# Kernel optimization log

Measured on AMD Instinct MI355X. Metric: run time of the kernel, lower is better.

The kernel has to match this reference:

```python
import math
import jax, jax.numpy as jnp
import numpy as np

B, S, D = 4, 2048, 512
N_HEADS, D_HEAD = 8, 64
NUM_BUCKETS, MAX_DIST = 32, 128


def _relative_position_bucket(relative_position, num_buckets=NUM_BUCKETS, max_distance=MAX_DIST):
    # bidirectional variant (is_decoder=False)
    num_buckets = num_buckets // 2
    rel_buckets = (relative_position > 0).astype(jnp.int32) * num_buckets
    rp = jnp.abs(relative_position)
    max_exact = num_buckets // 2
    is_small = rp < max_exact
    rp_large = max_exact + (
        jnp.log(rp.astype(jnp.float32) / max_exact)
        / math.log(max_distance / max_exact)
        * (num_buckets - max_exact)
    ).astype(jnp.int32)
    rp_large = jnp.minimum(rp_large, num_buckets - 1)
    return rel_buckets + jnp.where(is_small, rp, rp_large)


def compute_bias(rel_bias, q_len, k_len):
    ctx = jnp.arange(q_len)[:, None]
    mem = jnp.arange(k_len)[None, :]
    buckets = _relative_position_bucket(mem - ctx)           # [q, k]
    values = rel_bias[buckets]                                # [q, k, h]
    return jnp.transpose(values, (2, 0, 1))[None]             # [1, h, q, k]


def setup_inputs() -> dict:
    key = jax.random.key(0)
    ks = jax.random.split(key, 6)
    scale = 1.0 / math.sqrt(D)
    return {
        "hidden_states": jax.random.normal(ks[0], (B, S, D), jnp.float32),
        "Wq": jax.random.normal(ks[1], (D, D), jnp.float32) * scale,
        "Wk": jax.random.normal(ks[2], (D, D), jnp.float32) * scale,
        "Wv": jax.random.normal(ks[3], (D, D), jnp.float32) * scale,
        "Wo": jax.random.normal(ks[4], (D, D), jnp.float32) * scale,
        "rel_bias": jax.random.normal(ks[5], (NUM_BUCKETS, N_HEADS), jnp.float32),
    }


def reference(hidden_states, Wq, Wk, Wv, Wo, rel_bias):
    b, s, _ = hidden_states.shape
    # projections (no bias, no 1/sqrt(d) scaling — T5 style)
    q = (hidden_states @ Wq).reshape(b, s, N_HEADS, D_HEAD).transpose(0, 2, 1, 3)
    k = (hidden_states @ Wk).reshape(b, s, N_HEADS, D_HEAD).transpose(0, 2, 1, 3)
    v = (hidden_states @ Wv).reshape(b, s, N_HEADS, D_HEAD).transpose(0, 2, 1, 3)
    scores = jnp.einsum("bhqd,bhkd->bhqk", q, k)             # [b,h,s,s]
    position_bias = compute_bias(rel_bias, s, s)              # [1,h,s,s]
    scores = scores + position_bias
    attn = jax.nn.softmax(scores, axis=-1)                    # dropout: eval mode -> identity
    out = jnp.einsum("bhqk,bhkd->bhqd", attn, v)
    out = out.transpose(0, 2, 1, 3).reshape(b, s, N_HEADS * D_HEAD)
    return out @ Wo
```

## Files before the change

kernel.cpp:

```cpp
#include <hip/hip_runtime.h>
#include <stdint.h>

typedef __attribute__((ext_vector_type(8))) __bf16 bf16x8;
typedef __attribute__((ext_vector_type(4))) __bf16 bf16x4;
typedef __attribute__((ext_vector_type(8))) _Float16 f16x8;
typedef __attribute__((ext_vector_type(4))) float f32x4;
typedef __attribute__((ext_vector_type(4))) unsigned int u32x4;

#define SEQ 2048
#define LOG2E 1.4426950408889634f

#define OFF_AO    0ull
#define OFF_WF    8388608ull
#define OFF_WO    9961472ull
#define OFF_Q     10485760ull
#define OFF_K     18874368ull
#define OFF_VT    27262976ull
#define OFF_BIAS  35651584ull

__device__ __forceinline__ int swz(int row) { return ((row & 7) << 4) ^ ((row & 8) << 1); }

__device__ __forceinline__ void gl_lds16(const void* g, void* l) {
  __builtin_amdgcn_global_load_lds(
      (__attribute__((address_space(1))) void*)(uintptr_t)g,
      (__attribute__((address_space(3))) void*)(uint32_t)(uintptr_t)l, 16, 0, 0);
}

__device__ __forceinline__ float fast_exp2(float x) { return __builtin_amdgcn_exp2f(x); }

__global__ void k_prep(const float* __restrict__ Wq, const float* __restrict__ Wk,
                       const float* __restrict__ Wv, const float* __restrict__ Wo,
                       const float* __restrict__ rel_bias,
                       _Float16* __restrict__ wf, __bf16* __restrict__ wo_t,
                       float* __restrict__ bias_tab) {
  int z = blockIdx.z;
  __shared__ float tile[64][65];
  const float* W = (z == 0) ? Wq : (z == 1) ? Wk : (z == 2) ? Wv : Wo;
  int k0 = blockIdx.y * 64, n0 = blockIdx.x * 64;
  int tx = threadIdx.x & 63, ty = threadIdx.x >> 6;
  for (int r = ty; r < 64; r += 4) tile[r][tx] = W[(size_t)(k0 + r) * 512 + n0 + tx];
  __syncthreads();
  if (z < 3) {
    float scale = (z == 0) ? LOG2E : 1.0f;
    for (int r = ty; r < 64; r += 4)
      wf[(size_t)(z * 512 + n0 + r) * 512 + k0 + tx] = (_Float16)(tile[tx][r] * scale);
  } else {
    for (int r = ty; r < 64; r += 4)
      wo_t[(size_t)(n0 + r) * 512 + k0 + tx] = (__bf16)tile[tx][r];
    int blk = blockIdx.y * 8 + blockIdx.x;
#pragma unroll
    for (int e = 0; e < 2; ++e) {
      int idx = blk * 512 + e * 256 + threadIdx.x;
      int h = idx >> 12, dIdx = idx & 4095;
      float v = 0.f;
      if (dIdx < 4095) {
        int d = dIdx - 2047;
        int rp = d < 0 ? -d : d;
        int bp;
        if (rp < 8) bp = rp;
        else bp = 8 + (rp >= 12) + (rp >= 16) + (rp >= 23) + (rp >= 32) + (rp >= 46) + (rp >= 64) + (rp >= 91);
        v = rel_bias[((d > 0 ? 16 : 0) + bp) * 8 + h] * LOG2E;
      }
      bias_tab[idx] = v;
    }
  }
}

template <int MODE, int KSTEPS, int LDA, int LDB>
__global__ __launch_bounds__(256) void k_gemm(const void* __restrict__ Ap,
                                              const void* __restrict__ Btp,
                                              _Float16* __restrict__ qf,
                                              _Float16* __restrict__ kf,
                                              __bf16* __restrict__ vt,
                                              float* __restrict__ fo) {
  __shared__ __align__(16) char As[2][128 * 32 * 2];
  __shared__ __align__(16) char Bs[2][128 * 32 * 2];
  int tid = threadIdx.x, w = tid >> 6, l = tid & 63;
  int lr = l & 15, lh = l >> 4;
  int nwg = gridDim.x * gridDim.y;
  int flat = blockIdx.y * gridDim.x + blockIdx.x;
  int flat2 = (flat & 7) * (nwg >> 3) + (flat >> 3);
  int m0 = (flat2 / gridDim.x) * 128, n0 = (flat2 % gridDim.x) * 128;
  int wm = (w >> 1) * 64, wn = (w & 1) * 64;
  f32x4 zero4 = {0.f, 0.f, 0.f, 0.f};
  f32x4 acc[4][4];
#pragma unroll
  for (int i = 0; i < 4; ++i)
#pragma unroll
    for (int j = 0; j < 4; ++j) acc[i][j] = zero4;

  auto stage = [&](int kt, int buf) {
    if (MODE == 0) {
      const float* Af = (const float*)Ap;
#pragma unroll
      for (int c = 0; c < 2; ++c) {
        int i = c * 256 + tid;
        int row = i >> 2, cc = i & 3;
        const float* src = Af + (size_t)(m0 + row) * LDA + kt * 32 + cc * 8;
        float4 a = *(const float4*)src, b2 = *(const float4*)(src + 4);
        f16x8 hv;
        hv[0] = (_Float16)a.x;  hv[1] = (_Float16)a.y;
        hv[2] = (_Float16)a.z;  hv[3] = (_Float16)a.w;
        hv[4] = (_Float16)b2.x; hv[5] = (_Float16)b2.y;
        hv[6] = (_Float16)b2.z; hv[7] = (_Float16)b2.w;
        *(f16x8*)&As[buf][i * 16] = hv;
      }
#pragma unroll
      for (int c = 0; c < 2; ++c) {
        int i = c * 256 + tid;
        int row = i >> 2, cc = i & 3;
        gl_lds16((const char*)Btp + ((size_t)(n0 + row) * LDB + kt * 32 + cc * 8) * 2,
                 &Bs[buf][i * 16]);
      }
    } else {
#pragma unroll
      for (int c = 0; c < 2; ++c) {
        int i = c * 256 + tid;
        int row = i >> 2, cc = i & 3;
        gl_lds16((const char*)Ap + ((size_t)(m0 + row) * LDA + kt * 32 + cc * 8) * 2,
                 &As[buf][i * 16]);
        gl_lds16((const char*)Btp + ((size_t)(n0 + row) * LDB + kt * 32 + cc * 8) * 2,
                 &Bs[buf][i * 16]);
      }
    }
  };

  stage(0, 0);
  __syncthreads();
#pragma unroll 2
  for (int kt = 0; kt < KSTEPS; ++kt) {
    int cur = kt & 1;
    if (kt + 1 < KSTEPS) stage(kt + 1, cur ^ 1);
    u32x4 af[4], bfr[4];
#pragma unroll
    for (int mi = 0; mi < 4; ++mi)
      af[mi] = *(const u32x4*)&As[cur][((wm + mi * 16 + lr) * 32 + lh * 8) * 2];
#pragma unroll
    for (int ni = 0; ni < 4; ++ni)
      bfr[ni] = *(const u32x4*)&Bs[cur][((wn + ni * 16 + lr) * 32 + lh * 8) * 2];
#pragma unroll
    for (int mi = 0; mi < 4; ++mi)
#pragma unroll
      for (int ni = 0; ni < 4; ++ni) {
        if (MODE == 0)
          acc[mi][ni] = __builtin_amdgcn_mfma_f32_16x16x32_f16(
              __builtin_bit_cast(f16x8, af[mi]), __builtin_bit_cast(f16x8, bfr[ni]),
              acc[mi][ni], 0, 0, 0);
        else
          acc[mi][ni] = __builtin_amdgcn_mfma_f32_16x16x32_bf16(
              __builtin_bit_cast(bf16x8, af[mi]), __builtin_bit_cast(bf16x8, bfr[ni]),
              acc[mi][ni], 0, 0, 0);
      }
    __syncthreads();
  }

  if (MODE == 0 && n0 >= 1024) {
#pragma unroll
    for (int mi = 0; mi < 4; ++mi)
#pragma unroll
      for (int ni = 0; ni < 4; ++ni) {
        int m = m0 + wm + mi * 16 + lh * 4;
        int n = n0 + wn + ni * 16 + lr;
        int c9 = n & 511, hh = c9 >> 6, dh = c9 & 63;
        int b = m >> 11, s = m & 2047;
        int loc = s & 63;
        int pp = ((loc >> 5) << 5) | (((loc >> 2) & 3) << 3) | (((loc >> 4) & 1) << 2);
        bf16x4 o;
#pragma unroll
        for (int r = 0; r < 4; ++r) o[r] = (__bf16)acc[mi][ni][r];
        *(bf16x4*)&vt[((size_t)(b * 8 + hh) * 64 + dh) * 2048 + (s & ~63) + pp] = o;
      }
    return;
  }

#pragma unroll
  for (int mi = 0; mi < 4; ++mi)
#pragma unroll
    for (int ni = 0; ni < 4; ++ni)
#pragma unroll
      for (int r = 0; r < 4; ++r) {
        int m = m0 + wm + mi * 16 + lh * 4 + r;
        int n = n0 + wn + ni * 16 + lr;
        float vv = acc[mi][ni][r];
        if (MODE == 0) {
          int which = n >> 9, c9 = n & 511, hh = c9 >> 6, dh = c9 & 63;
          int b = m >> 11, s = m & 2047;
          size_t o = (size_t)((b * 8 + hh) * 2048 + s) * 64 + dh;
          if (which == 0) qf[o] = (_Float16)vv;
          else            kf[o] = (_Float16)vv;
        } else {
          fo[(size_t)m * 512 + n] = vv;
        }
      }
}

__global__ __launch_bounds__(512) void k_attn(const _Float16* __restrict__ qfp,
                                              const _Float16* __restrict__ kfp,
                                              const __bf16* __restrict__ vt,
                                              const float* __restrict__ bias_tab,
                                              __bf16* __restrict__ ao) {
  __shared__ __align__(16) char Ks[4][64 * 128];
  __shared__ __align__(16) char Vs[4][64 * 128];
  __shared__ float bias_s[2304];
  int tid = threadIdx.x, w = tid >> 6, l = tid & 63;
  int lr = l & 15, lh = l >> 4;
  int d = blockIdx.x;
  int bh = (d & 7) + ((d >> 3) & 3) * 8;
  int q0 = (d >> 5) * 256;
  int h = bh & 7, b = bh >> 3;
  const char* kbase = (const char*)(kfp + (size_t)bh * SEQ * 64);
  const char* vbase = (const char*)(vt + (size_t)bh * 64 * SEQ);

  float bR = bias_tab[h * 4096 + 2047 + 200];
  float bL = bias_tab[h * 4096 + 2047 - 200];

  for (int j = tid; j < 2304; j += 512)
    bias_s[j] = bias_tab[h * 4096 + (1792 - q0) + j];

  auto stageKV = [&](int kt, int buf) {
    const char* kb = kbase + (size_t)kt * 64 * 128;
    const char* vb = vbase + (size_t)kt * 128;
    int row = tid >> 3, colb = (tid & 7) * 16;
    gl_lds16(kb + row * 128 + (colb ^ swz(row)), &Ks[buf][tid * 16]);
    gl_lds16(vb + (size_t)row * 4096 + (colb ^ swz(row)), &Vs[buf][tid * 16]);
  };

  f16x8 qf[2][2];
#pragma unroll
  for (int qs = 0; qs < 2; ++qs) {
    int qrow = w * 32 + qs * 16 + lr;
    const _Float16* qg = qfp + ((size_t)bh * SEQ + q0 + qrow) * 64;
    qf[qs][0] = *(const f16x8*)(qg + lh * 8);
    qf[qs][1] = *(const f16x8*)(qg + 32 + lh * 8);
  }

  float l_run0 = 0.f, l_run1 = 0.f;
  f32x4 zero4 = {0.f, 0.f, 0.f, 0.f};
  f32x4 oacc[2][4];
#pragma unroll
  for (int qs = 0; qs < 2; ++qs)
#pragma unroll
    for (int i = 0; i < 4; ++i) oacc[qs][i] = zero4;

  auto qk = [&](int kt, int buf, f32x4 (&sacc)[2][4]) {
    int dmin = kt * 64 - q0 - 255, dmax = kt * 64 + 63 - q0;
    bool far = (dmin >= 91) || (dmax <= -91);
    f32x4 cinit[2][4];
    if (far) {
      float cb = (dmin >= 91) ? bR : bL;
#pragma unroll
      for (int qs = 0; qs < 2; ++qs)
#pragma unroll
        for (int t = 0; t < 4; ++t)
#pragma unroll
          for (int r = 0; r < 4; ++r) cinit[qs][t][r] = cb;
    } else {
#pragma unroll
      for (int qs = 0; qs < 2; ++qs) {
        int jb = kt * 64 + lh * 4 + 255 - (w * 32 + qs * 16 + lr);
#pragma unroll
        for (int t = 0; t < 4; ++t)
#pragma unroll
          for (int r = 0; r < 4; ++r) cinit[qs][t][r] = bias_s[jb + t * 16 + r];
      }
    }
    const char* kb = &Ks[buf][0];
    __builtin_amdgcn_s_setprio(1);
#pragma unroll
    for (int t = 0; t < 4; ++t) {
      int row = t * 16 + lr;
      f16x8 b0 = *(const f16x8*)(kb + row * 128 + ((lh * 16) ^ swz(row)));
      f16x8 b1 = *(const f16x8*)(kb + row * 128 + ((64 + lh * 16) ^ swz(row)));
#pragma unroll
      for (int qs = 0; qs < 2; ++qs) {
        f32x4 z = cinit[qs][t];
        z = __builtin_amdgcn_mfma_f32_16x16x32_f16(b0, qf[qs][0], z, 0, 0, 0);
        z = __builtin_amdgcn_mfma_f32_16x16x32_f16(b1, qf[qs][1], z, 0, 0, 0);
        sacc[qs][t] = z;
      }
    }
    __builtin_amdgcn_s_setprio(0);
  };

  auto finish = [&](int buf, f32x4 (&sacc)[2][4]) {
    bf16x8 paA[2], paB[2];
#pragma unroll
    for (int qs = 0; qs < 2; ++qs) {
      float p[4][4];
      float rt[4];
#pragma unroll
      for (int t = 0; t < 4; ++t) {
#pragma unroll
        for (int r = 0; r < 4; ++r) p[t][r] = fast_exp2(sacc[qs][t][r]);
        rt[t] = (p[t][0] + p[t][1]) + (p[t][2] + p[t][3]);
      }
      if (qs == 0) l_run0 += (rt[0] + rt[1]) + (rt[2] + rt[3]);
      else         l_run1 += (rt[0] + rt[1]) + (rt[2] + rt[3]);
      uint32_t pk[4][2];
#pragma unroll
      for (int t = 0; t < 4; ++t) {
        asm("v_cvt_pk_bf16_f32 %0, %1, %2" : "=v"(pk[t][0]) : "v"(p[t][0]), "v"(p[t][1]));
        asm("v_cvt_pk_bf16_f32 %0, %1, %2" : "=v"(pk[t][1]) : "v"(p[t][2]), "v"(p[t][3]));
      }
      u32x4 A0 = {pk[0][0], pk[0][1], pk[1][0], pk[1][1]};
      u32x4 A1 = {pk[2][0], pk[2][1], pk[3][0], pk[3][1]};
      paA[qs] = __builtin_bit_cast(bf16x8, A0);
      paB[qs] = __builtin_bit_cast(bf16x8, A1);
    }
    const char* vbr = &Vs[buf][0];
    __builtin_amdgcn_s_setprio(1);
#pragma unroll
    for (int ni = 0; ni < 4; ++ni) {
      int vrow = ni * 16 + lr;
      bf16x8 v0 = *(const bf16x8*)(vbr + vrow * 128 + ((lh * 16) ^ swz(vrow)));
      bf16x8 v1 = *(const bf16x8*)(vbr + vrow * 128 + ((64 + lh * 16) ^ swz(vrow)));
#pragma unroll
      for (int qs = 0; qs < 2; ++qs) {
        oacc[qs][ni] = __builtin_amdgcn_mfma_f32_16x16x32_bf16(paA[qs], v0, oacc[qs][ni], 0, 0, 0);
        oacc[qs][ni] = __builtin_amdgcn_mfma_f32_16x16x32_bf16(paB[qs], v1, oacc[qs][ni], 0, 0, 0);
      }
    }
    __builtin_amdgcn_s_setprio(0);
  };

  stageKV(0, 0);
  stageKV(1, 1);
  __syncthreads();
  f32x4 sA[2][4], sB[2][4];
#pragma unroll 2
  for (int kp = 0; kp < 16; ++kp) {
    int rb_ = (kp & 1) * 2;
    qk(2 * kp, rb_, sA);
    qk(2 * kp + 1, rb_ + 1, sB);
    if (kp < 15) {
      stageKV(2 * kp + 2, rb_ ^ 2);
      stageKV(2 * kp + 3, (rb_ ^ 2) + 1);
    }
    finish(rb_, sA);
    finish(rb_ + 1, sB);
    __syncthreads();
  }

  l_run0 += __shfl_xor(l_run0, 16);
  l_run0 += __shfl_xor(l_run0, 32);
  l_run1 += __shfl_xor(l_run1, 16);
  l_run1 += __shfl_xor(l_run1, 32);

#pragma unroll
  for (int qs = 0; qs < 2; ++qs) {
    float lsel = (qs == 0) ? l_run0 : l_run1;
#pragma unroll
    for (int r = 0; r < 4; ++r) {
      float linv = 1.0f / __shfl(lsel, lh * 4 + r);
      int s = q0 + w * 32 + qs * 16 + lh * 4 + r;
#pragma unroll
      for (int ni = 0; ni < 4; ++ni) {
        int dh = ni * 16 + lr;
        ao[((size_t)(b * 2048 + s)) * 512 + h * 64 + dh] = (__bf16)(oacc[qs][ni][r] * linv);
      }
    }
  }
}

extern "C" void kernel_launch(void* const* d_in, const int* in_sizes, int n_in,
                              void* d_out, int out_size, void* d_ws, size_t ws_size,
                              hipStream_t stream) {
  (void)in_sizes; (void)n_in; (void)out_size; (void)ws_size;
  const float* hs = (const float*)d_in[0];
  const float* Wq = (const float*)d_in[1];
  const float* Wk = (const float*)d_in[2];
  const float* Wv = (const float*)d_in[3];
  const float* Wo = (const float*)d_in[4];
  const float* rb = (const float*)d_in[5];
  char* ws = (char*)d_ws;
  _Float16* wfb  = (_Float16*)(ws + OFF_WF);
  __bf16* wo_t   = (__bf16*)(ws + OFF_WO);
  _Float16* qfb  = (_Float16*)(ws + OFF_Q);
  _Float16* kfb  = (_Float16*)(ws + OFF_K);
  __bf16* vtb    = (__bf16*)(ws + OFF_VT);
  __bf16* aob    = (__bf16*)(ws + OFF_AO);
  float*  bias   = (float*)(ws + OFF_BIAS);

  k_prep<<<dim3(8, 8, 4), 256, 0, stream>>>(Wq, Wk, Wv, Wo, rb, wfb, wo_t, bias);
  k_gemm<0, 16, 512, 512><<<dim3(12, 64), 256, 0, stream>>>(hs, wfb, qfb, kfb, vtb, nullptr);
  k_attn<<<dim3(256), 512, 0, stream>>>(qfb, kfb, vtb, bias, aob);
  k_gemm<1, 16, 512, 512><<<dim3(4, 64), 256, 0, stream>>>(aob, wo_t, nullptr, nullptr, nullptr, (float*)d_out);
}
```

Measured before the change: 87.03 us.

## Deepen attention K/V staging to four tiles and narrow output GEMM tiles

The attention kernel now keeps 8 K/V LDS buffers and processes four key tiles per barrier, prefetching the next group of four tiles. This halves the number of __syncthreads and raises prefetch depth, at the cost of doubling K/V shared memory, which may lower occupancy. Separately, the output projection GEMM uses 128x64 tiles with twice as many workgroups (512) to spread the small GEMM across more CUs.

New measurement: 131.7 us. +51.3%, slower.

```diff
diff --git a/kernel.cpp b/kernel.cpp
--- a/kernel.cpp
+++ b/kernel.cpp
@@ -80,14 +80,17 @@
   int nwg = gridDim.x * gridDim.y;
   int flat = blockIdx.y * gridDim.x + blockIdx.x;
   int flat2 = (flat & 7) * (nwg >> 3) + (flat >> 3);
-  int m0 = (flat2 / gridDim.x) * 128, n0 = (flat2 % gridDim.x) * 128;
-  int wm = (w >> 1) * 64, wn = (w & 1) * 64;
+  constexpr int NTW = (MODE == 0) ? 128 : 64;
+  constexpr int NI = (MODE == 0) ? 4 : 2;
+  int m0 = (flat2 / gridDim.x) * 128, n0 = (flat2 % gridDim.x) * NTW;
+  int wm = (w >> 1) * 64;
+  int wn = (MODE == 0) ? (w & 1) * 64 : (w & 1) * 32;
   f32x4 zero4 = {0.f, 0.f, 0.f, 0.f};
-  f32x4 acc[4][4];
+  f32x4 acc[4][NI];
 #pragma unroll
   for (int i = 0; i < 4; ++i)
 #pragma unroll
-    for (int j = 0; j < 4; ++j) acc[i][j] = zero4;
+    for (int j = 0; j < NI; ++j) acc[i][j] = zero4;
 
   auto stage = [&](int kt, int buf) {
     if (MODE == 0) {
@@ -119,6 +122,10 @@
         int row = i >> 2, cc = i & 3;
         gl_lds16((const char*)Ap + ((size_t)(m0 + row) * LDA + kt * 32 + cc * 8) * 2,
                  &As[buf][i * 16]);
+      }
+      {
+        int i = tid;
+        int row = i >> 2, cc = i & 3;
         gl_lds16((const char*)Btp + ((size_t)(n0 + row) * LDB + kt * 32 + cc * 8) * 2,
                  &Bs[buf][i * 16]);
       }
@@ -131,17 +138,17 @@
   for (int kt = 0; kt < KSTEPS; ++kt) {
     int cur = kt & 1;
     if (kt + 1 < KSTEPS) stage(kt + 1, cur ^ 1);
-    u32x4 af[4], bfr[4];
+    u32x4 af[4], bfr[NI];
 #pragma unroll
     for (int mi = 0; mi < 4; ++mi)
       af[mi] = *(const u32x4*)&As[cur][((wm + mi * 16 + lr) * 32 + lh * 8) * 2];
 #pragma unroll
-    for (int ni = 0; ni < 4; ++ni)
+    for (int ni = 0; ni < NI; ++ni)
       bfr[ni] = *(const u32x4*)&Bs[cur][((wn + ni * 16 + lr) * 32 + lh * 8) * 2];
 #pragma unroll
     for (int mi = 0; mi < 4; ++mi)
 #pragma unroll
-      for (int ni = 0; ni < 4; ++ni) {
+      for (int ni = 0; ni < NI; ++ni) {
         if (MODE == 0)
           acc[mi][ni] = __builtin_amdgcn_mfma_f32_16x16x32_f16(
               __builtin_bit_cast(f16x8, af[mi]), __builtin_bit_cast(f16x8, bfr[ni]),
@@ -158,7 +165,7 @@
 #pragma unroll
     for (int mi = 0; mi < 4; ++mi)
 #pragma unroll
-      for (int ni = 0; ni < 4; ++ni) {
+      for (int ni = 0; ni < NI; ++ni) {
         int m = m0 + wm + mi * 16 + lh * 4;
         int n = n0 + wn + ni * 16 + lr;
         int c9 = n & 511, hh = c9 >> 6, dh = c9 & 63;
@@ -176,7 +183,7 @@
 #pragma unroll
   for (int mi = 0; mi < 4; ++mi)
 #pragma unroll
-    for (int ni = 0; ni < 4; ++ni)
+    for (int ni = 0; ni < NI; ++ni)
 #pragma unroll
       for (int r = 0; r < 4; ++r) {
         int m = m0 + wm + mi * 16 + lh * 4 + r;
@@ -199,8 +206,8 @@
                                               const __bf16* __restrict__ vt,
                                               const float* __restrict__ bias_tab,
                                               __bf16* __restrict__ ao) {
-  __shared__ __align__(16) char Ks[4][64 * 128];
-  __shared__ __align__(16) char Vs[4][64 * 128];
+  __shared__ __align__(16) char Ks[8][64 * 128];
+  __shared__ __align__(16) char Vs[8][64 * 128];
   __shared__ float bias_s[2304];
   int tid = threadIdx.x, w = tid >> 6, l = tid & 63;
   int lr = l & 15, lh = l >> 4;
@@ -325,19 +332,29 @@
 
   stageKV(0, 0);
   stageKV(1, 1);
+  stageKV(2, 2);
+  stageKV(3, 3);
   __syncthreads();
   f32x4 sA[2][4], sB[2][4];
 #pragma unroll 2
-  for (int kp = 0; kp < 16; ++kp) {
-    int rb_ = (kp & 1) * 2;
-    qk(2 * kp, rb_, sA);
-    qk(2 * kp + 1, rb_ + 1, sB);
-    if (kp < 15) {
-      stageKV(2 * kp + 2, rb_ ^ 2);
-      stageKV(2 * kp + 3, (rb_ ^ 2) + 1);
-    }
-    finish(rb_, sA);
+  for (int kp = 0; kp < 8; ++kp) {
+    int rb_ = (kp & 1) * 4;
+    qk(4 * kp, rb_ + 0, sA);
+    qk(4 * kp + 1, rb_ + 1, sB);
+    if (kp < 7) {
+      stageKV(4 * kp + 4, (rb_ ^ 4) + 0);
+      stageKV(4 * kp + 5, (rb_ ^ 4) + 1);
+    }
+    finish(rb_ + 0, sA);
     finish(rb_ + 1, sB);
+    qk(4 * kp + 2, rb_ + 2, sA);
+    qk(4 * kp + 3, rb_ + 3, sB);
+    if (kp < 7) {
+      stageKV(4 * kp + 6, (rb_ ^ 4) + 2);
+      stageKV(4 * kp + 7, (rb_ ^ 4) + 3);
+    }
+    finish(rb_ + 2, sA);
+    finish(rb_ + 3, sB);
     __syncthreads();
   }
 
@@ -384,5 +401,5 @@
   k_prep<<<dim3(8, 8, 4), 256, 0, stream>>>(Wq, Wk, Wv, Wo, rb, wfb, wo_t, bias);
   k_gemm<0, 16, 512, 512><<<dim3(12, 64), 256, 0, stream>>>(hs, wfb, qfb, kfb, vtb, nullptr);
   k_attn<<<dim3(256), 512, 0, stream>>>(qfb, kfb, vtb, bias, aob);
-  k_gemm<1, 16, 512, 512><<<dim3(4, 64), 256, 0, stream>>>(aob, wo_t, nullptr, nullptr, nullptr, (float*)d_out);
+  k_gemm<1, 16, 512, 512><<<dim3(8, 64), 256, 0, stream>>>(aob, wo_t, nullptr, nullptr, nullptr, (float*)d_out);
 }
```
